# Kernel tuning notes

Measured on AMD Instinct MI355X. Metric: run time of the kernel, lower is better.

Reference implementation:

```python
import jax, jax.numpy as jnp
import numpy as np
from jax import lax

B, T, P, CF, ED, NHID = 32, 8192, 16, 4, 32, 64
CD = ED * (P // CF)            # 128 = code_dim
K, NHEADS, NLAYERS, DFF = 1024, 4, 4, 256
DH = CD // NHEADS
NEG = -1e9


def conv1d(x, w, b, stride=1, pad=0):
    # x: [N, Cin, L], w: [Cout, Cin, k]
    y = lax.conv_general_dilated(x, w, (stride,), [(pad, pad)],
                                 dimension_numbers=("NCH", "OIH", "NCH"))
    return y + b[None, :, None]


def layernorm(x, g, b, eps=1e-5):
    m = jnp.mean(x, -1, keepdims=True)
    v = jnp.mean((x - m) ** 2, -1, keepdims=True)
    return (x - m) * lax.rsqrt(v + eps) * g + b


def setup_inputs() -> dict:
    key = jax.random.key(0)
    ks = iter(jax.random.split(key, 40))
    n = lambda shape, s=0.02: jax.random.normal(next(ks), shape, jnp.float32) * s
    return {
        "x": jax.random.normal(next(ks), (B, T, 1), jnp.float32),
        "enc_w1": n((NHID // 2, 1, 4)), "enc_b1": jnp.zeros((NHID // 2,), jnp.float32),
        "enc_w2": n((NHID, NHID // 2, 4)), "enc_b2": jnp.zeros((NHID,), jnp.float32),
        "enc_w3": n((NHID, NHID, 3)), "enc_b3": jnp.zeros((NHID,), jnp.float32),
        "res_w1": n((2, 32, NHID, 3)), "res_b1": jnp.zeros((2, 32), jnp.float32),
        "res_w2": n((2, NHID, 32, 1)), "res_b2": jnp.zeros((2, NHID), jnp.float32),
        "pre_w": n((ED, NHID, 1)), "pre_b": jnp.zeros((ED,), jnp.float32),
        "codebook": jax.random.uniform(next(ks), (K, CD), jnp.float32, -1.0 / K, 1.0 / K),
        "pos_emb": n((512, CD)),
        "qkv_w": n((NLAYERS, 3 * CD, CD)), "qkv_b": jnp.zeros((NLAYERS, 3 * CD), jnp.float32),
        "proj_w": n((NLAYERS, CD, CD)), "proj_b": jnp.zeros((NLAYERS, CD), jnp.float32),
        "ln1_g": jnp.ones((NLAYERS, CD), jnp.float32), "ln1_b": jnp.zeros((NLAYERS, CD), jnp.float32),
        "ln2_g": jnp.ones((NLAYERS, CD), jnp.float32), "ln2_b": jnp.zeros((NLAYERS, CD), jnp.float32),
        "ffn_w1": n((NLAYERS, DFF, CD)), "ffn_b1": jnp.zeros((NLAYERS, DFF), jnp.float32),
        "ffn_w2": n((NLAYERS, CD, DFF)), "ffn_b2": jnp.zeros((NLAYERS, CD), jnp.float32),
        "fin_g": jnp.ones((CD,), jnp.float32), "fin_b": jnp.zeros((CD,), jnp.float32),
        "head_w": n((K, CD)), "head_b": jnp.zeros((K,), jnp.float32),
    }


def reference(x, enc_w1, enc_b1, enc_w2, enc_b2, enc_w3, enc_b3,
              res_w1, res_b1, res_w2, res_b2, pre_w, pre_b,
              codebook, pos_emb, qkv_w, qkv_b, proj_w, proj_b,
              ln1_g, ln1_b, ln2_g, ln2_b, ffn_w1, ffn_b1, ffn_w2, ffn_b2,
              fin_g, fin_b, head_w, head_b):
    Bx, Tx, C = x.shape
    npatch = Tx // P
    # [B, T, 1] -> patches, channel-major per patch -> [N, 1, P]
    xp = x[:, :npatch * P, :].reshape(Bx, npatch, P, C)
    xp = xp.transpose(0, 1, 3, 2).reshape(-1, 1, P)
    h = jax.nn.relu(conv1d(xp, enc_w1, enc_b1, stride=2, pad=1))
    h = jax.nn.relu(conv1d(h, enc_w2, enc_b2, stride=2, pad=1))
    h = conv1d(h, enc_w3, enc_b3, stride=1, pad=1)
    for i in range(res_w1.shape[0]):           # fixed 2 residual layers
        t = conv1d(jax.nn.relu(h), res_w1[i], res_b1[i], stride=1, pad=1)
        t = conv1d(jax.nn.relu(t), res_w2[i], res_b2[i], stride=1, pad=0)
        h = h + t
    h = jax.nn.relu(h)
    z = conv1d(h, pre_w, pre_b)                # [N, ED, P//CF]
    z_flat = z.reshape(z.shape[0], -1)         # [N, CD]
    # --- flattened VQ: squared-dist + argmin + straight-through ---
    d = (jnp.sum(z_flat ** 2, 1, keepdims=True) + jnp.sum(codebook ** 2, 1)
         - 2.0 * (z_flat @ codebook.T))        # [N, K]
    idx = jnp.argmin(d, axis=1)
    q = codebook[idx]
    sg = lax.stop_gradient
    e_loss = jnp.mean((sg(q) - z_flat) ** 2)
    q_loss = jnp.mean((q - sg(z_flat)) ** 2)
    vq_loss = q_loss + 0.25 * e_loss
    q_st = z_flat + sg(q - z_flat)
    # --- causal transformer over quantized codes ---
    S = npatch
    hh = q_st.reshape(Bx, S, CD) + pos_emb[:S][None]
    mask = jnp.where(jnp.triu(jnp.ones((S, S), bool), k=1), NEG, 0.0).astype(hh.dtype)
    scale = 1.0 / jnp.sqrt(jnp.asarray(DH, hh.dtype))
    for i in range(NLAYERS):
        qkv = hh @ qkv_w[i].T + qkv_b[i]
        qh, kh, vh = [t.reshape(Bx, S, NHEADS, DH) for t in jnp.split(qkv, 3, -1)]
        scores = jnp.einsum("bqhd,bkhd->bhqk", qh, kh) * scale + mask
        attn = jax.nn.softmax(scores, -1)
        o = jnp.einsum("bhqk,bkhd->bqhd", attn, vh).reshape(Bx, S, CD)
        o = o @ proj_w[i].T + proj_b[i]
        hh = layernorm(hh + o, ln1_g[i], ln1_b[i])
        f = jax.nn.gelu(hh @ ffn_w1[i].T + ffn_b1[i], approximate=False)
        f = f @ ffn_w2[i].T + ffn_b2[i]
        hh = layernorm(hh + f, ln2_g[i], ln2_b[i])
    hh = layernorm(hh, fin_g, fin_b)
    logits = hh @ head_w.T + head_b            # [B, S, K]
    return logits, vq_loss, idx.reshape(Bx, S)
```

## Files before the change

kernel.cpp:

```cpp
#include <hip/hip_runtime.h>
#include <math.h>

#define NPATCH 16384
#define SEQ    512
#define LOSS_OFF 16777216
#define IDX_OFF  16777217

typedef short bf8 __attribute__((ext_vector_type(8)));
typedef _Float16 h8 __attribute__((ext_vector_type(8)));
typedef float f32x4 __attribute__((ext_vector_type(4)));

__device__ inline short f2bf(float x) {
  unsigned u = __float_as_uint(x);
  u += 0x7fffu + ((u >> 16) & 1u);
  return (short)(u >> 16);
}
__device__ inline float bf2f(short h) {
  return __uint_as_float(((unsigned)(unsigned short)h) << 16);
}

__device__ inline void splitf16(float v, short& hi, short& lo) {
  _Float16 h = (fabsf(v) < 6.1035156e-5f) ? (_Float16)0.f : (_Float16)v;
  hi = __builtin_bit_cast(short, h);
  lo = __builtin_bit_cast(short, (_Float16)((v - (float)h) * 4096.f));
}

#define EW2_OFF 0
#define EW3_OFF 8192
#define ERA_OFF 20480
#define ERB_OFF 32768
#define EPW_OFF 36864
#define EWTOT   38912

__global__ __launch_bounds__(256) void enc_split(
    const float* __restrict__ w2, const float* __restrict__ w3,
    const float* __restrict__ rw1, const float* __restrict__ rw2,
    const float* __restrict__ pw,
    unsigned short* __restrict__ eh, unsigned short* __restrict__ el) {
  int i = blockIdx.x * 256 + threadIdx.x;
  float v;
  if (i < 8192) {
    int t = i >> 11, co = (i >> 5) & 63, ci = i & 31;
    v = w2[(co * 32 + ci) * 4 + t];
  } else if (i < 20480) {
    int j = i - 8192;
    int t = j >> 12, co = (j >> 6) & 63, ci = j & 63;
    v = w3[(co * 64 + ci) * 3 + t];
  } else if (i < 32768) {
    int j = i - 20480;
    int rl = j / 6144; j -= rl * 6144;
    int t = j >> 11, co = (j >> 6) & 31, ci = j & 63;
    v = rw1[((rl * 32 + co) * 64 + ci) * 3 + t];
  } else if (i < 36864) {
    int j = i - 32768;
    int rl = j >> 11, co = (j >> 5) & 63, ci = j & 31;
    v = rw2[(rl * 64 + co) * 32 + ci];
  } else {
    int j = i - 36864;
    int co = j >> 6, ci = j & 63;
    v = pw[co * 64 + ci];
  }
  short hh_, ll_;
  splitf16(v, hh_, ll_);
  eh[i] = (unsigned short)hh_;
  el[i] = (unsigned short)ll_;
}

__global__ __launch_bounds__(256) void cb_split(
    const float* __restrict__ cb, unsigned short* __restrict__ ch,
    unsigned short* __restrict__ cl, float* __restrict__ cn) {
  const int i = blockIdx.x * 256 + threadIdx.x;
  float v = cb[i];
  short hi, lo;
  splitf16(v * 64.f, hi, lo);
  ch[i] = (unsigned short)hi;
  cl[i] = (unsigned short)lo;
  float s = v * v;
#pragma unroll
  for (int o = 1; o < 64; o <<= 1) s += __shfl_xor(s, o);
  __shared__ float red[4];
  if ((threadIdx.x & 63) == 0) red[threadIdx.x >> 6] = s;
  __syncthreads();
  if (threadIdx.x == 0)   cn[i >> 7] = red[0] + red[1];
  if (threadIdx.x == 128) cn[i >> 7] = red[2] + red[3];
}

#define H1P 2624
#define H2P 2304
__global__ __launch_bounds__(256, 4) void encoder7(
    const float* __restrict__ x,
    const float* __restrict__ w1, const float* __restrict__ b1,
    const float* __restrict__ b2, const float* __restrict__ b3,
    const float* __restrict__ rb1, const float* __restrict__ rb2,
    const float* __restrict__ pb,
    const unsigned short* __restrict__ ewh, const unsigned short* __restrict__ ewl,
    float* __restrict__ z, unsigned short* __restrict__ zh,
    unsigned short* __restrict__ zl) {
  __shared__ __align__(16) short arena[9856];
  short* H1h = arena;
  short* H1l = arena + H1P;
  short* H2h = arena + 2 * H1P;
  short* H2l = arena + 2 * H1P + H2P;
  short* T1h = arena;
  short* T1l = arena + 1280;
  float* XS  = (float*)(arena + 2 * H1P);

  const int tid = threadIdx.x;
  const int wave = tid >> 6, lane = tid & 63, quad = lane >> 4, l15 = lane & 15;
  const int mt = wave >> 1, nh = wave & 1;
  const size_t pbase = (size_t)blockIdx.x * 8;
  const h8 zh8 = {0, 0, 0, 0, 0, 0, 0, 0};
  const f32x4 zf4 = {0.f, 0.f, 0.f, 0.f};

  h8 w2h[4][2], w2l[4][2];
#pragma unroll
  for (int t = 0; t < 4; ++t)
#pragma unroll
    for (int j = 0; j < 2; ++j) {
      const int wb = EW2_OFF + (t * 64 + (nh * 2 + j) * 16 + l15) * 32 + quad * 8;
      w2h[t][j] = *reinterpret_cast<const h8*>(ewh + wb);
      w2l[t][j] = *reinterpret_cast<const h8*>(ewl + wb);
    }

  if (tid < 32) {
    int pp = tid >> 2, i = (tid & 3) * 4;
    *reinterpret_cast<float4*>(&XS[pp * 16 + i]) =
        *reinterpret_cast<const float4*>(x + (pbase + pp) * 16 + i);
  }
  __syncthreads();

  {
    const int pp = tid >> 5, op = (tid >> 2) & 7, qt = tid & 3;
    float xv[4];
#pragma unroll
    for (int kk = 0; kk < 4; ++kk) {
      int ip = 2 * op + kk - 1;
      xv[kk] = (ip >= 0 && ip < 16) ? XS[pp * 16 + ip] : 0.f;
    }
    bf8 sh, sl;
#pragma unroll
    for (int c = 0; c < 8; ++c) {
      int co = qt * 8 + c;
      float4 wv = *reinterpret_cast<const float4*>(w1 + co * 4);
      float a = b1[co] + xv[0] * wv.x + xv[1] * wv.y + xv[2] * wv.z + xv[3] * wv.w;
      a = fmaxf(a, 0.f);
      short hs, ls;
      splitf16(a, hs, ls);
      sh[c] = hs; sl[c] = ls;
    }
    const int off = pp * 328 + op * 40 + qt * 8;
    *reinterpret_cast<bf8*>(&H1h[off]) = sh;
    *reinterpret_cast<bf8*>(&H1l[off]) = sl;
  }
  __syncthreads();

  f32x4 h3keep[2];

  f32x4 acc2A[2] = {zf4, zf4};
  f32x4 acc2B[2] = {zf4, zf4};
  {
    const float bs2_0 = b2[nh * 32 + l15];
    const float bs2_1 = b2[nh * 32 + 16 + l15];
    const int patch = mt * 4 + (l15 >> 2), outp = l15 & 3;
#pragma unroll
    for (int t = 0; t < 4; ++t) {
      const int ip = 2 * outp + t - 1;
      const bool vld = (unsigned)ip < 8u;
      const int aoff = patch * 328 + (vld ? ip : 0) * 40 + quad * 8;
      h8 ah = *reinterpret_cast<const h8*>(&H1h[aoff]);
      h8 al = *reinterpret_cast<const h8*>(&H1l[aoff]);
      if (!vld) { ah = zh8; al = zh8; }
#pragma unroll
      for (int j = 0; j < 2; ++j) {
        acc2A[j] = __builtin_amdgcn_mfma_f32_16x16x32_f16(ah, w2h[t][j], acc2A[j], 0, 0, 0);
        acc2B[j] = __builtin_amdgcn_mfma_f32_16x16x32_f16(ah, w2l[t][j], acc2B[j], 0, 0, 0);
        acc2B[j] = __builtin_amdgcn_mfma_f32_16x16x32_f16(al, w2h[t][j], acc2B[j], 0, 0, 0);
      }
    }
    h8 w3h[3][2][2], w3l[3][2][2];
#pragma unroll
    for (int t = 0; t < 3; ++t)
#pragma unroll
      for (int ks = 0; ks < 2; ++ks)
#pragma unroll
        for (int j = 0; j < 2; ++j) {
          const int wb = EW3_OFF + (t * 64 + (nh * 2 + j) * 16 + l15) * 64 + ks * 32 + quad * 8;
          w3h[t][ks][j] = *reinterpret_cast<const h8*>(ewh + wb);
          w3l[t][ks][j] = *reinterpret_cast<const h8*>(ewl + wb);
        }
#pragma unroll
    for (int j = 0; j < 2; ++j) {
      const int col = (nh * 2 + j) * 16 + l15;
      const float bs = (j == 0) ? bs2_0 : bs2_1;
#pragma unroll
      for (int r = 0; r < 4; ++r) {
        float v = fmaxf(acc2A[j][r] + acc2B[j][r] * (1.f / 4096.f) + bs, 0.f);
        short vh, vl;
        splitf16(v, vh, vl);
        const int m = mt * 16 + quad * 4 + r;
        H2h[m * 72 + col] = vh;
        H2l[m * 72 + col] = vl;
      }
    }
    __syncthreads();

    f32x4 accA[2] = {zf4, zf4};
    f32x4 accB[2] = {zf4, zf4};
    const float bs3_0 = b3[nh * 32 + l15];
    const float bs3_1 = b3[nh * 32 + 16 + l15];
    const int pos = l15 & 3;
#pragma unroll
    for (int t = 0; t < 3; ++t) {
      const int ip = pos + t - 1;
      const bool vld = (unsigned)ip < 4u;
      const int row = patch * 4 + (vld ? ip : 0);
#pragma unroll
      for (int ks = 0; ks < 2; ++ks) {
        const int aoff = row * 72 + ks * 32 + quad * 8;
        h8 ah = *reinterpret_cast<const h8*>(&H2h[aoff]);
        h8 al = *reinterpret_cast<const h8*>(&H2l[aoff]);
        if (!vld) { ah = zh8; al = zh8; }
#pragma unroll
        for (int j = 0; j < 2; ++j) {
          accA[j] = __builtin_amdgcn_mfma_f32_16x16x32_f16(ah, w3h[t][ks][j], accA[j], 0, 0, 0);
          accB[j] = __builtin_amdgcn_mfma_f32_16x16x32_f16(ah, w3l[t][ks][j], accB[j], 0, 0, 0);
          accB[j] = __builtin_amdgcn_mfma_f32_16x16x32_f16(al, w3h[t][ks][j], accB[j], 0, 0, 0);
        }
      }
    }
    __syncthreads();
#pragma unroll
    for (int j = 0; j < 2; ++j) {
      const int col = (nh * 2 + j) * 16 + l15;
      const float bs = (j == 0) ? bs3_0 : bs3_1;
#pragma unroll
      for (int r = 0; r < 4; ++r) {
        float v = accA[j][r] + accB[j][r] * (1.f / 4096.f) + bs;
        h3keep[j][r] = v;
        short vh, vl;
        splitf16(fmaxf(v, 0.f), vh, vl);
        const int m = mt * 16 + quad * 4 + r;
        H2h[m * 72 + col] = vh;
        H2l[m * 72 + col] = vl;
      }
    }
  }
  __syncthreads();

  for (int rl = 0; rl < 2; ++rl) {
    {
      h8 wah[3][2], wal[3][2];
#pragma unroll
      for (int t = 0; t < 3; ++t)
#pragma unroll
        for (int ks = 0; ks < 2; ++ks) {
          const int wb = ERA_OFF + ((rl * 3 + t) * 32 + nh * 16 + l15) * 64 + ks * 32 + quad * 8;
          wah[t][ks] = *reinterpret_cast<const h8*>(ewh + wb);
          wal[t][ks] = *reinterpret_cast<const h8*>(ewl + wb);
        }
      const float bsa = rb1[rl * 32 + nh * 16 + l15];
      f32x4 accA = zf4, accB = zf4;
      const int patch = mt * 4 + (l15 >> 2), pos = l15 & 3;
#pragma unroll
      for (int t = 0; t < 3; ++t) {
        const int ip = pos + t - 1;
        const bool vld = (unsigned)ip < 4u;
        const int row = patch * 4 + (vld ? ip : 0);
#pragma unroll
        for (int ks = 0; ks < 2; ++ks) {
          const int aoff = row * 72 + ks * 32 + quad * 8;
          h8 ah = *reinterpret_cast<const h8*>(&H2h[aoff]);
          h8 al = *reinterpret_cast<const h8*>(&H2l[aoff]);
          if (!vld) { ah = zh8; al = zh8; }
          accA = __builtin_amdgcn_mfma_f32_16x16x32_f16(ah, wah[t][ks], accA, 0, 0, 0);
          accB = __builtin_amdgcn_mfma_f32_16x16x32_f16(ah, wal[t][ks], accB, 0, 0, 0);
          accB = __builtin_amdgcn_mfma_f32_16x16x32_f16(al, wah[t][ks], accB, 0, 0, 0);
        }
      }
      const int col = nh * 16 + l15;
#pragma unroll
      for (int r = 0; r < 4; ++r) {
        float v = fmaxf(accA[r] + accB[r] * (1.f / 4096.f) + bsa, 0.f);
        short vh, vl;
        splitf16(v, vh, vl);
        const int m = mt * 16 + quad * 4 + r;
        T1h[m * 40 + col] = vh;
        T1l[m * 40 + col] = vl;
      }
    }
    __syncthreads();
    {
      h8 wbh[2], wbl[2];
#pragma unroll
      for (int j = 0; j < 2; ++j) {
        const int wb = ERB_OFF + (rl * 64 + (nh * 2 + j) * 16 + l15) * 32 + quad * 8;
        wbh[j] = *reinterpret_cast<const h8*>(ewh + wb);
        wbl[j] = *reinterpret_cast<const h8*>(ewl + wb);
      }
      const float bsb0 = rb2[rl * 64 + nh * 32 + l15];
      const float bsb1 = rb2[rl * 64 + nh * 32 + 16 + l15];
      f32x4 accA[2] = {zf4, zf4};
      f32x4 accB[2] = {zf4, zf4};
      const int aoff = (mt * 16 + l15) * 40 + quad * 8;
      h8 ah = *reinterpret_cast<const h8*>(&T1h[aoff]);
      h8 al = *reinterpret_cast<const h8*>(&T1l[aoff]);
#pragma unroll
      for (int j = 0; j < 2; ++j) {
        accA[j] = __builtin_amdgcn_mfma_f32_16x16x32_f16(ah, wbh[j], accA[j], 0, 0, 0);
        accB[j] = __builtin_amdgcn_mfma_f32_16x16x32_f16(ah, wbl[j], accB[j], 0, 0, 0);
        accB[j] = __builtin_amdgcn_mfma_f32_16x16x32_f16(al, wbh[j], accB[j], 0, 0, 0);
      }
#pragma unroll
      for (int j = 0; j < 2; ++j) {
        const int col = (nh * 2 + j) * 16 + l15;
        const float bs = (j == 0) ? bsb0 : bsb1;
#pragma unroll
        for (int r = 0; r < 4; ++r) {
          float v = h3keep[j][r] + accA[j][r] + accB[j][r] * (1.f / 4096.f) + bs;
          h3keep[j][r] = v;
          short vh, vl;
          splitf16(fmaxf(v, 0.f), vh, vl);
          const int m = mt * 16 + quad * 4 + r;
          H2h[m * 72 + col] = vh;
          H2l[m * 72 + col] = vl;
        }
      }
    }
    __syncthreads();
  }

  {
    h8 wph[2], wpl[2];
#pragma unroll
    for (int ks = 0; ks < 2; ++ks) {
      const int wb = EPW_OFF + (nh * 16 + l15) * 64 + ks * 32 + quad * 8;
      wph[ks] = *reinterpret_cast<const h8*>(ewh + wb);
      wpl[ks] = *reinterpret_cast<const h8*>(ewl + wb);
    }
    const float bs = pb[nh * 16 + l15];
    f32x4 accA = zf4, accB = zf4;
    const int arow = mt * 16 + l15;
#pragma unroll
    for (int ks = 0; ks < 2; ++ks) {
      const int aoff = arow * 72 + ks * 32 + quad * 8;
      h8 ah = *reinterpret_cast<const h8*>(&H2h[aoff]);
      h8 al = *reinterpret_cast<const h8*>(&H2l[aoff]);
      accA = __builtin_amdgcn_mfma_f32_16x16x32_f16(ah, wph[ks], accA, 0, 0, 0);
      accB = __builtin_amdgcn_mfma_f32_16x16x32_f16(ah, wpl[ks], accB, 0, 0, 0);
      accB = __builtin_amdgcn_mfma_f32_16x16x32_f16(al, wph[ks], accB, 0, 0, 0);
    }
    const int pn = mt * 4 + quad;
    const int col = nh * 16 + l15;
    float ov[4];
#pragma unroll
    for (int r = 0; r < 4; ++r) ov[r] = accA[r] + accB[r] * (1.f / 4096.f) + bs;
    const size_t off = (pbase + pn) * 128 + col * 4;
    *reinterpret_cast<float4*>(z + off) = *reinterpret_cast<float4*>(ov);
    ushort4 h4, l4;
    unsigned short* hp = (unsigned short*)&h4;
    unsigned short* lp = (unsigned short*)&l4;
#pragma unroll
    for (int r = 0; r < 4; ++r) {
      short vh, vl;
      splitf16(ov[r] * 256.f, vh, vl);
      hp[r] = (unsigned short)vh;
      lp[r] = (unsigned short)vl;
    }
    *reinterpret_cast<ushort4*>(&zh[off]) = h4;
    *reinterpret_cast<ushort4*>(&zl[off]) = l4;
  }
}

__global__ __launch_bounds__(256) void cast_w(
    const float* __restrict__ qkv_w, const float* __restrict__ proj_w,
    const float* __restrict__ f1, const float* __restrict__ f2,
    const float* __restrict__ hw, unsigned short* __restrict__ wb) {
  int i = blockIdx.x * 256 + threadIdx.x;
  float v;
  if (i < 196608) v = qkv_w[i];
  else if (i < 262144) v = proj_w[i - 196608];
  else if (i < 393216) v = f1[i - 262144];
  else if (i < 524288) v = f2[i - 393216];
  else v = hw[i - 524288];
  wb[i] = (unsigned short)f2bf(v);
}

__global__ __launch_bounds__(256) void vq_argmin3(
    const unsigned short* __restrict__ Ahg, const unsigned short* __restrict__ Alg,
    const unsigned short* __restrict__ Bhg, const unsigned short* __restrict__ Blg,
    const float* __restrict__ cbf, unsigned long long* __restrict__ keys) {
  __shared__ short Ah[128 * 40], Al[128 * 40], Bh[64 * 40], Bl[64 * 40];
  __shared__ float cns[64];
  const int tid = threadIdx.x;
  const int n0 = blockIdx.x * 64, m0 = blockIdx.y * 128;
  const int wave = tid >> 6, lane = tid & 63, quad = lane >> 4, l15 = lane & 15;
  const f32x4 z4 = {0.f, 0.f, 0.f, 0.f};
  f32x4 accA[2][4], accB[2][4];
#pragma unroll
  for (int i = 0; i < 2; ++i)
#pragma unroll
    for (int j = 0; j < 4; ++j) { accA[i][j] = z4; accB[i][j] = z4; }
  {
    const int lr = tid >> 2, q = tid & 3;
    const float4* bp = reinterpret_cast<const float4*>(cbf + (size_t)(n0 + lr) * 128 + q * 32);
    float s = 0.f;
#pragma unroll
    for (int e = 0; e < 8; ++e) {
      float4 v = bp[e];
      s += v.x * v.x + v.y * v.y + v.z * v.z + v.w * v.w;
    }
    s += __shfl_xor(s, 1); s += __shfl_xor(s, 2);
    if (q == 0) cns[lr] = s;
  }
  const int ra = tid >> 1, ha = (tid & 1) * 16;
  const int rb = tid >> 2, hb = (tid & 3) * 8;
  for (int k0 = 0; k0 < 128; k0 += 32) {
    {
      const size_t abase = (size_t)(m0 + ra) * 128 + k0 + ha;
      *reinterpret_cast<bf8*>(&Ah[ra * 40 + ha])     = *reinterpret_cast<const bf8*>(&Ahg[abase]);
      *reinterpret_cast<bf8*>(&Ah[ra * 40 + ha + 8]) = *reinterpret_cast<const bf8*>(&Ahg[abase + 8]);
      *reinterpret_cast<bf8*>(&Al[ra * 40 + ha])     = *reinterpret_cast<const bf8*>(&Alg[abase]);
      *reinterpret_cast<bf8*>(&Al[ra * 40 + ha + 8]) = *reinterpret_cast<const bf8*>(&Alg[abase + 8]);
      const size_t bbase = (size_t)(n0 + rb) * 128 + k0 + hb;
      *reinterpret_cast<bf8*>(&Bh[rb * 40 + hb]) = *reinterpret_cast<const bf8*>(&Bhg[bbase]);
      *reinterpret_cast<bf8*>(&Bl[rb * 40 + hb]) = *reinterpret_cast<const bf8*>(&Blg[bbase]);
    }
    __syncthreads();
    h8 af[2], afl[2], bfh[4], bfl[4];
#pragma unroll
    for (int mt = 0; mt < 2; ++mt) {
      int row = wave * 32 + mt * 16 + l15;
      af[mt]  = *reinterpret_cast<const h8*>(&Ah[row * 40 + quad * 8]);
      afl[mt] = *reinterpret_cast<const h8*>(&Al[row * 40 + quad * 8]);
    }
#pragma unroll
    for (int nt = 0; nt < 4; ++nt) {
      int row = nt * 16 + l15;
      bfh[nt] = *reinterpret_cast<const h8*>(&Bh[row * 40 + quad * 8]);
      bfl[nt] = *reinterpret_cast<const h8*>(&Bl[row * 40 + quad * 8]);
    }
#pragma unroll
    for (int nt = 0; nt < 4; ++nt)
#pragma unroll
      for (int mt = 0; mt < 2; ++mt) {
        accA[mt][nt] = __builtin_amdgcn_mfma_f32_16x16x32_f16(af[mt], bfh[nt], accA[mt][nt], 0, 0, 0);
        accB[mt][nt] = __builtin_amdgcn_mfma_f32_16x16x32_f16(af[mt], bfl[nt], accB[mt][nt], 0, 0, 0);
        accB[mt][nt] = __builtin_amdgcn_mfma_f32_16x16x32_f16(afl[mt], bfh[nt], accB[mt][nt], 0, 0, 0);
      }
    __syncthreads();
  }
#pragma unroll
  for (int mt = 0; mt < 2; ++mt)
#pragma unroll
    for (int r = 0; r < 4; ++r) {
      const int row = m0 + wave * 32 + mt * 16 + quad * 4 + r;
      unsigned long long key = ~0ull;
#pragma unroll
      for (int nt = 0; nt < 4; ++nt) {
        const int c16 = nt * 16 + l15;
        float s = (accA[mt][nt][r] + accB[mt][nt][r] * (1.f / 4096.f)) * (1.f / 16384.f);
        float dv = cns[c16] - 2.f * s;
        unsigned u = __float_as_uint(dv);
        u = (u & 0x80000000u) ? ~u : (u | 0x80000000u);
        unsigned long long k = ((unsigned long long)u << 32) | (unsigned)(n0 + c16);
        key = k < key ? k : key;
      }
#pragma unroll
      for (int off = 1; off < 16; off <<= 1) {
        unsigned long long o = __shfl_xor(key, off);
        key = o < key ? o : key;
      }
      if (l15 == 0) atomicMin(&keys[row], key);
    }
}

__global__ __launch_bounds__(256) void vq_gather3(
    const float* __restrict__ z, const float* __restrict__ cb,
    const float* __restrict__ pos, const unsigned long long* __restrict__ keys,
    float* __restrict__ hh, unsigned short* __restrict__ hh_b,
    float* __restrict__ lpart, float* __restrict__ idx_out) {
  const int blk = blockIdx.x, tid = threadIdx.x;
  __shared__ int sidx[8];
  if (tid < 8) {
    unsigned long long k = keys[blk * 8 + tid];
    int id = (int)(unsigned)(k & 0xffffffffull);
    sidx[tid] = id;
    idx_out[blk * 8 + tid] = (float)id;
  }
  __syncthreads();
  const int p = tid >> 5, d = tid & 31;
  const size_t n = (size_t)blk * 8 + p;
  const int idx = sidx[p];
  float4 q = *reinterpret_cast<const float4*>(cb + (size_t)idx * 128 + d * 4);
  float4 zv = *reinterpret_cast<const float4*>(z + n * 128 + d * 4);
  float4 pv = *reinterpret_cast<const float4*>(pos + (size_t)(n & 511) * 128 + d * 4);
  float hv[4] = {q.x + pv.x, q.y + pv.y, q.z + pv.z, q.w + pv.w};
  *reinterpret_cast<float4*>(hh + n * 128 + d * 4) = *reinterpret_cast<float4*>(hv);
  ushort4 h4;
  unsigned short* hp = (unsigned short*)&h4;
#pragma unroll
  for (int e = 0; e < 4; ++e) hp[e] = (unsigned short)f2bf(hv[e]);
  *reinterpret_cast<ushort4*>(&hh_b[n * 128 + d * 4]) = h4;
  float dx = q.x - zv.x, dy = q.y - zv.y, dz = q.z - zv.z, dw = q.w - zv.w;
  float part = dx * dx + dy * dy + dz * dz + dw * dw;
#pragma unroll
  for (int o = 1; o < 64; o <<= 1) part += __shfl_xor(part, o);
  __shared__ float lred[4];
  if ((tid & 63) == 0) lred[tid >> 6] = part;
  __syncthreads();
  if (tid == 0) lpart[blk] = lred[0] + lred[1] + lred[2] + lred[3];
}

template <int ACT, int SPLIT>
__global__ __launch_bounds__(256) void mgemm_b64(
    const unsigned short* __restrict__ Ag, const unsigned short* __restrict__ Bg,
    const float* __restrict__ bias, float* __restrict__ C,
    unsigned short* __restrict__ Cb, int N) {
  __shared__ short Ah[64 * 40], Bh[64 * 40];
  const int tid = threadIdx.x;
  const int n0 = blockIdx.x * 64, m0 = blockIdx.y * 64;
  const int wave = tid >> 6, lane = tid & 63, quad = lane >> 4, l15 = lane & 15;
  const f32x4 z4 = {0.f, 0.f, 0.f, 0.f};
  f32x4 acc[4] = {z4, z4, z4, z4};

  const int ra = tid >> 2, ha = (tid & 3) * 8;
  for (int k0 = 0; k0 < 128; k0 += 32) {
    *reinterpret_cast<bf8*>(&Ah[ra * 40 + ha]) =
        *reinterpret_cast<const bf8*>(&Ag[(size_t)(m0 + ra) * 128 + k0 + ha]);
    *reinterpret_cast<bf8*>(&Bh[ra * 40 + ha]) =
        *reinterpret_cast<const bf8*>(&Bg[(size_t)(n0 + ra) * 128 + k0 + ha]);
    __syncthreads();
    bf8 af = *reinterpret_cast<const bf8*>(&Ah[(wave * 16 + l15) * 40 + quad * 8]);
    bf8 bfh[4];
#pragma unroll
    for (int nt = 0; nt < 4; ++nt)
      bfh[nt] = *reinterpret_cast<const bf8*>(&Bh[(nt * 16 + l15) * 40 + quad * 8]);
#pragma unroll
    for (int nt = 0; nt < 4; ++nt)
      acc[nt] = __builtin_amdgcn_mfma_f32_16x16x32_bf16(af, bfh[nt], acc[nt], 0, 0, 0);
    __syncthreads();
  }
#pragma unroll
  for (int nt = 0; nt < 4; ++nt) {
    int col = n0 + nt * 16 + l15;
    float bv = bias[col];
    int rbase = m0 + wave * 16 + quad * 4;
#pragma unroll
    for (int r = 0; r < 4; ++r) {
      float v = acc[nt][r] + bv;
      if (ACT == 1) v = 0.5f * v * (1.f + erff(v * 0.7071067811865476f));
      if (SPLIT) Cb[(size_t)(rbase + r) * N + col] = (unsigned short)f2bf(v);
      else       C[(size_t)(rbase + r) * N + col] = v;
    }
  }
}

template <int K, int FINAL>
__global__ __launch_bounds__(256) void mgemm_ln3(
    const unsigned short* __restrict__ Ag, const unsigned short* __restrict__ Bg,
    const float* __restrict__ bias, const float* __restrict__ res,
    const float* __restrict__ g, const float* __restrict__ bb,
    const float* __restrict__ g2, const float* __restrict__ bb2,
    float* __restrict__ C, unsigned short* __restrict__ Cb) {
  __shared__ short Ah[16 * 40], Bh[128 * 40];
  __shared__ float red1[16][4], red2[16][4], red3[16][4], red4[16][4];
  const int tid = threadIdx.x;
  const int m0 = blockIdx.x * 16;
  const int wave = tid >> 6, lane = tid & 63, quad = lane >> 4, l15 = lane & 15;
  const f32x4 z4 = {0.f, 0.f, 0.f, 0.f};
  f32x4 acc[2] = {z4, z4};

  const int rb = tid >> 1, hb = (tid & 1) * 16;
  for (int k0 = 0; k0 < K; k0 += 32) {
    if (tid < 64) {
      const int ra = tid >> 2, ha = (tid & 3) * 8;
      *reinterpret_cast<bf8*>(&Ah[ra * 40 + ha]) =
          *reinterpret_cast<const bf8*>(&Ag[(size_t)(m0 + ra) * K + k0 + ha]);
    }
    {
      const size_t bbase = (size_t)rb * K + k0 + hb;
      *reinterpret_cast<bf8*>(&Bh[rb * 40 + hb])     = *reinterpret_cast<const bf8*>(&Bg[bbase]);
      *reinterpret_cast<bf8*>(&Bh[rb * 40 + hb + 8]) = *reinterpret_cast<const bf8*>(&Bg[bbase + 8]);
    }
    __syncthreads();
    bf8 af = *reinterpret_cast<const bf8*>(&Ah[l15 * 40 + quad * 8]);
#pragma unroll
    for (int j = 0; j < 2; ++j) {
      bf8 bf = *reinterpret_cast<const bf8*>(&Bh[(wave * 32 + j * 16 + l15) * 40 + quad * 8]);
      acc[j] = __builtin_amdgcn_mfma_f32_16x16x32_bf16(af, bf, acc[j], 0, 0, 0);
    }
    __syncthreads();
  }
  float bias_v[2], g_v[2], bb_v[2], g2_v[2], bb2_v[2];
#pragma unroll
  for (int j = 0; j < 2; ++j) {
    const int col = wave * 32 + j * 16 + l15;
    bias_v[j] = bias[col]; g_v[j] = g[col]; bb_v[j] = bb[col];
    if (FINAL) { g2_v[j] = g2[col]; bb2_v[j] = bb2[col]; }
  }
  float ov[4][2];
#pragma unroll
  for (int r = 0; r < 4; ++r) {
    const int row = m0 + quad * 4 + r;
#pragma unroll
    for (int j = 0; j < 2; ++j)
      ov[r][j] = acc[j][r] + bias_v[j] +
                 res[(size_t)row * 128 + wave * 32 + j * 16 + l15];
    float s = ov[r][0] + ov[r][1];
    s += __shfl_xor(s, 1); s += __shfl_xor(s, 2);
    s += __shfl_xor(s, 4); s += __shfl_xor(s, 8);
    if (l15 == 0) red1[quad * 4 + r][wave] = s;
  }
  __syncthreads();
  float mean[4];
#pragma unroll
  for (int r = 0; r < 4; ++r) {
    const int lr = quad * 4 + r;
    mean[r] = (red1[lr][0] + red1[lr][1] + red1[lr][2] + red1[lr][3]) * 0.0078125f;
  }
#pragma unroll
  for (int r = 0; r < 4; ++r) {
    float s2 = 0.f;
#pragma unroll
    for (int j = 0; j < 2; ++j) { ov[r][j] -= mean[r]; s2 += ov[r][j] * ov[r][j]; }
    s2 += __shfl_xor(s2, 1); s2 += __shfl_xor(s2, 2);
    s2 += __shfl_xor(s2, 4); s2 += __shfl_xor(s2, 8);
    if (l15 == 0) red2[quad * 4 + r][wave] = s2;
  }
  __syncthreads();
  float rstd[4];
#pragma unroll
  for (int r = 0; r < 4; ++r) {
    const int lr = quad * 4 + r;
    rstd[r] = rsqrtf((red2[lr][0] + red2[lr][1] + red2[lr][2] + red2[lr][3]) *
                     0.0078125f + 1e-5f);
  }
  if (FINAL) {
    float yv[4][2];
#pragma unroll
    for (int r = 0; r < 4; ++r) {
      float s3 = 0.f;
#pragma unroll
      for (int j = 0; j < 2; ++j) {
        yv[r][j] = ov[r][j] * rstd[r] * g_v[j] + bb_v[j];
        s3 += yv[r][j];
      }
      s3 += __shfl_xor(s3, 1); s3 += __shfl_xor(s3, 2);
      s3 += __shfl_xor(s3, 4); s3 += __shfl_xor(s3, 8);
      if (l15 == 0) red3[quad * 4 + r][wave] = s3;
    }
    __syncthreads();
    float mean2[4];
#pragma unroll
    for (int r = 0; r < 4; ++r) {
      const int lr = quad * 4 + r;
      mean2[r] = (red3[lr][0] + red3[lr][1] + red3[lr][2] + red3[lr][3]) * 0.0078125f;
    }
#pragma unroll
    for (int r = 0; r < 4; ++r) {
      float s4 = 0.f;
#pragma unroll
      for (int j = 0; j < 2; ++j) { yv[r][j] -= mean2[r]; s4 += yv[r][j] * yv[r][j]; }
      s4 += __shfl_xor(s4, 1); s4 += __shfl_xor(s4, 2);
      s4 += __shfl_xor(s4, 4); s4 += __shfl_xor(s4, 8);
      if (l15 == 0) red4[quad * 4 + r][wave] = s4;
    }
    __syncthreads();
#pragma unroll
    for (int r = 0; r < 4; ++r) {
      const int lr = quad * 4 + r;
      float rstd2 = rsqrtf((red4[lr][0] + red4[lr][1] + red4[lr][2] + red4[lr][3]) *
                           0.0078125f + 1e-5f);
      const int row = m0 + lr;
#pragma unroll
      for (int j = 0; j < 2; ++j) {
        float v = yv[r][j] * rstd2 * g2_v[j] + bb2_v[j];
        Cb[(size_t)row * 128 + wave * 32 + j * 16 + l15] = (unsigned short)f2bf(v);
      }
    }
  } else {
#pragma unroll
    for (int r = 0; r < 4; ++r) {
      const int row = m0 + quad * 4 + r;
#pragma unroll
      for (int j = 0; j < 2; ++j) {
        float v = ov[r][j] * rstd[r] * g_v[j] + bb_v[j];
        size_t off = (size_t)row * 128 + wave * 32 + j * 16 + l15;
        C[off] = v;
        Cb[off] = (unsigned short)f2bf(v);
      }
    }
  }
}

__global__ __launch_bounds__(256) void attn_b(
    const unsigned short* __restrict__ qb, unsigned short* __restrict__ ob) {
  const int qt = blockIdx.x, h = blockIdx.y, b = blockIdx.z;
  __shared__ short Kh[64 * 40];
  __shared__ short Vth[32 * 72];
  __shared__ float Ss[64 * 72];
  __shared__ float ms[64], ls[64], alphas[64];
  const int tid = threadIdx.x;
  const int wave = tid >> 6, lane = tid & 63, quad = lane >> 4, l15 = lane & 15;
  const size_t tbase = (size_t)b * 512 + qt * 64;
  bf8 qf;
  {
    const size_t qoff = (tbase + wave * 16 + l15) * 384 + h * 32 + quad * 8;
    qf = *reinterpret_cast<const bf8*>(&qb[qoff]);
  }
  if (tid < 64) { ms[tid] = -1e30f; ls[tid] = 0.f; }
  const f32x4 z4 = {0.f, 0.f, 0.f, 0.f};
  f32x4 o[2] = {z4, z4};
  const float scale = 0.17677669529663687f;
  const int sr = tid >> 2, sc8 = (tid & 3) * 8;
  for (int kt = 0; kt <= qt; ++kt) {
    const size_t kbase = (size_t)b * 512 + kt * 64;
    {
      const size_t koff = (kbase + sr) * 384 + 128 + h * 32 + sc8;
      *reinterpret_cast<bf8*>(&Kh[sr * 40 + sc8]) = *reinterpret_cast<const bf8*>(&qb[koff]);
      const size_t voff = (kbase + sr) * 384 + 256 + h * 32 + sc8;
      bf8 vh8 = *reinterpret_cast<const bf8*>(&qb[voff]);
#pragma unroll
      for (int j = 0; j < 8; ++j) Vth[(sc8 + j) * 72 + sr] = vh8[j];
    }
    __syncthreads();
    {
#pragma unroll
      for (int nt = 0; nt < 4; ++nt) {
        bf8 kf = *reinterpret_cast<const bf8*>(&Kh[(nt * 16 + l15) * 40 + quad * 8]);
        f32x4 s = __builtin_amdgcn_mfma_f32_16x16x32_bf16(qf, kf, z4, 0, 0, 0);
#pragma unroll
        for (int r = 0; r < 4; ++r) {
          int row64 = wave * 16 + quad * 4 + r;
          int col64 = nt * 16 + l15;
          float v = s[r] * scale;
          if (kt == qt && col64 > row64) v += -1e9f;
          Ss[row64 * 72 + col64] = v;
        }
      }
    }
    __syncthreads();
    {
      const int i = tid >> 2, q = tid & 3;
      float mx = -3.4e38f;
      float4 pv[4];
#pragma unroll
      for (int t = 0; t < 4; ++t) {
        pv[t] = *reinterpret_cast<const float4*>(&Ss[i * 72 + q * 16 + t * 4]);
        mx = fmaxf(mx, fmaxf(fmaxf(pv[t].x, pv[t].y), fmaxf(pv[t].z, pv[t].w)));
      }
      mx = fmaxf(mx, __shfl_xor(mx, 1));
      mx = fmaxf(mx, __shfl_xor(mx, 2));
      float mold = ms[i];
      mx = fmaxf(mx, mold);
      float sum = 0.f;
#pragma unroll
      for (int t = 0; t < 4; ++t) {
        pv[t].x = __expf(pv[t].x - mx); pv[t].y = __expf(pv[t].y - mx);
        pv[t].z = __expf(pv[t].z - mx); pv[t].w = __expf(pv[t].w - mx);
        sum += pv[t].x + pv[t].y + pv[t].z + pv[t].w;
        *reinterpret_cast<float4*>(&Ss[i * 72 + q * 16 + t * 4]) = pv[t];
      }
      sum += __shfl_xor(sum, 1);
      sum += __shfl_xor(sum, 2);
      if (q == 0) {
        float alpha = __expf(mold - mx);
        ls[i] = ls[i] * alpha + sum;
        ms[i] = mx;
        alphas[i] = alpha;
      }
    }
    __syncthreads();
    {
      bf8 ph[2];
#pragma unroll
      for (int c = 0; c < 2; ++c) {
        const float* pp = &Ss[(wave * 16 + l15) * 72 + c * 32 + quad * 8];
        float4 p0 = *reinterpret_cast<const float4*>(pp);
        float4 p1 = *reinterpret_cast<const float4*>(pp + 4);
        float pf[8] = {p0.x, p0.y, p0.z, p0.w, p1.x, p1.y, p1.z, p1.w};
#pragma unroll
        for (int j = 0; j < 8; ++j) ph[c][j] = f2bf(pf[j]);
      }
      float a0 = alphas[wave * 16 + quad * 4 + 0];
      float a1 = alphas[wave * 16 + quad * 4 + 1];
      float a2 = alphas[wave * 16 + quad * 4 + 2];
      float a3 = alphas[wave * 16 + quad * 4 + 3];
#pragma unroll
      for (int dt = 0; dt < 2; ++dt) {
        o[dt][0] *= a0; o[dt][1] *= a1; o[dt][2] *= a2; o[dt][3] *= a3;
#pragma unroll
        for (int c = 0; c < 2; ++c) {
          bf8 vf = *reinterpret_cast<const bf8*>(&Vth[(dt * 16 + l15) * 72 + c * 32 + quad * 8]);
          o[dt] = __builtin_amdgcn_mfma_f32_16x16x32_bf16(ph[c], vf, o[dt], 0, 0, 0);
        }
      }
    }
    __syncthreads();
  }
#pragma unroll
  for (int r = 0; r < 4; ++r) {
    float inv = 1.f / ls[wave * 16 + quad * 4 + r];
    size_t row = tbase + wave * 16 + quad * 4 + r;
#pragma unroll
    for (int dt = 0; dt < 2; ++dt) {
      float v = o[dt][r] * inv;
      ob[row * 128 + h * 32 + dt * 16 + l15] = (unsigned short)f2bf(v);
    }
  }
}

__global__ __launch_bounds__(256) void loss_finalize2(const float* __restrict__ lp,
                                                      float* __restrict__ out) {
  float s = 0.f;
  for (int i = threadIdx.x; i < 2048; i += 256) s += lp[i];
#pragma unroll
  for (int o = 1; o < 64; o <<= 1) s += __shfl_xor(s, o);
  __shared__ float red[4];
  if ((threadIdx.x & 63) == 0) red[threadIdx.x >> 6] = s;
  __syncthreads();
  if (threadIdx.x == 0)
    out[0] = 1.25f * (red[0] + red[1] + red[2] + red[3]) / 2097152.0f;
}

extern "C" void kernel_launch(void* const* d_in, const int* in_sizes, int n_in,
                              void* d_out, int out_size, void* d_ws, size_t ws_size,
                              hipStream_t stream) {
  const float* x      = (const float*)d_in[0];
  const float* enc_w1 = (const float*)d_in[1];
  const float* enc_b1 = (const float*)d_in[2];
  const float* enc_w2 = (const float*)d_in[3];
  const float* enc_b2 = (const float*)d_in[4];
  const float* enc_w3 = (const float*)d_in[5];
  const float* enc_b3 = (const float*)d_in[6];
  const float* res_w1 = (const float*)d_in[7];
  const float* res_b1 = (const float*)d_in[8];
  const float* res_w2 = (const float*)d_in[9];
  const float* res_b2 = (const float*)d_in[10];
  const float* pre_w  = (const float*)d_in[11];
  const float* pre_b  = (const float*)d_in[12];
  const float* codebook = (const float*)d_in[13];
  const float* pos_emb  = (const float*)d_in[14];
  const float* qkv_w  = (const float*)d_in[15];
  const float* qkv_b  = (const float*)d_in[16];
  const float* proj_w = (const float*)d_in[17];
  const float* proj_b = (const float*)d_in[18];
  const float* ln1_g  = (const float*)d_in[19];
  const float* ln1_b  = (const float*)d_in[20];
  const float* ln2_g  = (const float*)d_in[21];
  const float* ln2_b  = (const float*)d_in[22];
  const float* ffn_w1 = (const float*)d_in[23];
  const float* ffn_b1 = (const float*)d_in[24];
  const float* ffn_w2 = (const float*)d_in[25];
  const float* ffn_b2 = (const float*)d_in[26];
  const float* fin_g  = (const float*)d_in[27];
  const float* fin_b  = (const float*)d_in[28];
  const float* head_w = (const float*)d_in[29];
  const float* head_b = (const float*)d_in[30];

  float* out = (float*)d_out;
  float* ws  = (float*)d_ws;

  unsigned long long* keys = (unsigned long long*)ws;
  float* lpart = ws + 32768;
  unsigned short* wb = (unsigned short*)(ws + 36864);
  unsigned short* hhln_b = (unsigned short*)(ws + 692224);

  float* zf = out;
  float* hh = out + 2097152;
  unsigned short* hh_b   = (unsigned short*)(out + 4194304);
  unsigned short* qkvb_b = (unsigned short*)(out + 6291456);
  unsigned short* oatt_b = (unsigned short*)(out + 12582912);
  unsigned short* fbuf_b = (unsigned short*)(out + 0);

  unsigned short* ewh = (unsigned short*)(out + 6291456);
  unsigned short* ewl = ewh + EWTOT;

  unsigned short* zh = (unsigned short*)(out + 6340608);
  unsigned short* zl = (unsigned short*)(out + 7389184);
  unsigned short* cbh = (unsigned short*)(out + 12582912);
  unsigned short* cbl = (unsigned short*)(out + 12648448);
  float* cnbuf = out + 12713984;

  const int W_QKV = 0, W_PROJ = 196608, W_F1 = 262144, W_F2 = 393216, W_HEAD = 524288;

  hipMemsetAsync(keys, 0xFF, NPATCH * sizeof(unsigned long long), stream);

  enc_split<<<152, 256, 0, stream>>>(enc_w2, enc_w3, res_w1, res_w2, pre_w, ewh, ewl);
  cb_split<<<512, 256, 0, stream>>>(codebook, cbh, cbl, cnbuf);
  encoder7<<<2048, 256, 0, stream>>>(x, enc_w1, enc_b1, enc_b2, enc_b3,
                                     res_b1, res_b2, pre_b, ewh, ewl, zf, zh, zl);
  cast_w<<<2304, 256, 0, stream>>>(qkv_w, proj_w, ffn_w1, ffn_w2, head_w, wb);
  vq_argmin3<<<dim3(16, 128), 256, 0, stream>>>(zh, zl, cbh, cbl, codebook, keys);
  vq_gather3<<<2048, 256, 0, stream>>>(zf, codebook, pos_emb, keys, hh, hh_b,
                                       lpart, out + IDX_OFF);
  for (int i = 0; i < 4; ++i) {
    mgemm_b64<0, 1><<<dim3(6, 256), 256, 0, stream>>>(
        hh_b, wb + W_QKV + i * 49152, qkv_b + i * 384, nullptr, qkvb_b, 384);
    attn_b<<<dim3(8, 4, 32), 256, 0, stream>>>(qkvb_b, oatt_b);
    mgemm_ln3<128, 0><<<1024, 256, 0, stream>>>(
        oatt_b, wb + W_PROJ + i * 16384, proj_b + i * 128, hh,
        ln1_g + i * 128, ln1_b + i * 128, nullptr, nullptr, hh, hh_b);
    mgemm_b64<1, 1><<<dim3(4, 256), 256, 0, stream>>>(
        hh_b, wb + W_F1 + i * 32768, ffn_b1 + i * 256, nullptr, fbuf_b, 256);
    if (i < 3) {
      mgemm_ln3<256, 0><<<1024, 256, 0, stream>>>(
          fbuf_b, wb + W_F2 + i * 32768, ffn_b2 + i * 128, hh,
          ln2_g + i * 128, ln2_b + i * 128, nullptr, nullptr, hh, hh_b);
    } else {
      mgemm_ln3<256, 1><<<1024, 256, 0, stream>>>(
          fbuf_b, wb + W_F2 + i * 32768, ffn_b2 + i * 128, hh,
          ln2_g + i * 128, ln2_b + i * 128, fin_g, fin_b, hh, hhln_b);
    }
  }
  mgemm_b64<0, 0><<<dim3(16, 256), 256, 0, stream>>>(
      hhln_b, wb + W_HEAD, head_b, out, nullptr, 1024);
  loss_finalize2<<<1, 256, 0, stream>>>(lpart, out + LOSS_OFF);
}
```

Measured before the change: 538.8 us.

## Fuse FFN up/down GEMMs with LayerNorm and merge prep kernels

Replaces the separate FFN1 GEMM (with GELU) and FFN2+LayerNorm kernels with one kernel. Each 64-row tile keeps the GELU intermediate in shared memory, so the 256-wide activation never goes through global memory. It also folds the encoder weight split, codebook split, weight cast and key memset into one prep launch, and replaces the final loss reduction kernel with atomicAdd into the output. This cuts launches and global traffic, at the cost of fewer blocks per FFN launch (256), higher LDS use per block, and nondeterministic float atomic ordering in the loss.

```diff
diff --git a/kernel.cpp b/kernel.cpp
--- a/kernel.cpp
+++ b/kernel.cpp
@@ -32,57 +32,75 @@
 #define EPW_OFF 36864
 #define EWTOT   38912
 
-__global__ __launch_bounds__(256) void enc_split(
+__global__ __launch_bounds__(256) void prep_all(
     const float* __restrict__ w2, const float* __restrict__ w3,
     const float* __restrict__ rw1, const float* __restrict__ rw2,
-    const float* __restrict__ pw,
-    unsigned short* __restrict__ eh, unsigned short* __restrict__ el) {
-  int i = blockIdx.x * 256 + threadIdx.x;
-  float v;
-  if (i < 8192) {
-    int t = i >> 11, co = (i >> 5) & 63, ci = i & 31;
-    v = w2[(co * 32 + ci) * 4 + t];
-  } else if (i < 20480) {
-    int j = i - 8192;
-    int t = j >> 12, co = (j >> 6) & 63, ci = j & 63;
-    v = w3[(co * 64 + ci) * 3 + t];
-  } else if (i < 32768) {
-    int j = i - 20480;
-    int rl = j / 6144; j -= rl * 6144;
-    int t = j >> 11, co = (j >> 6) & 31, ci = j & 63;
-    v = rw1[((rl * 32 + co) * 64 + ci) * 3 + t];
-  } else if (i < 36864) {
-    int j = i - 32768;
-    int rl = j >> 11, co = (j >> 5) & 63, ci = j & 31;
-    v = rw2[(rl * 64 + co) * 32 + ci];
+    const float* __restrict__ pw, const float* __restrict__ cb,
+    const float* __restrict__ qkv_w, const float* __restrict__ proj_w,
+    const float* __restrict__ f1, const float* __restrict__ f2,
+    const float* __restrict__ hw,
+    unsigned short* __restrict__ eh, unsigned short* __restrict__ el,
+    unsigned short* __restrict__ cbh, unsigned short* __restrict__ cbl,
+    float* __restrict__ cn, unsigned short* __restrict__ wb,
+    unsigned long long* __restrict__ keys, float* __restrict__ loss_out) {
+  __shared__ float red[4];
+  const int b = blockIdx.x, tid = threadIdx.x;
+  if (b < 152) {
+    int i = b * 256 + tid;
+    float v;
+    if (i < 8192) {
+      int t = i >> 11, co = (i >> 5) & 63, ci = i & 31;
+      v = w2[(co * 32 + ci) * 4 + t];
+    } else if (i < 20480) {
+      int j = i - 8192;
+      int t = j >> 12, co = (j >> 6) & 63, ci = j & 63;
+      v = w3[(co * 64 + ci) * 3 + t];
+    } else if (i < 32768) {
+      int j = i - 20480;
+      int rl = j / 6144; j -= rl * 6144;
+      int t = j >> 11, co = (j >> 6) & 31, ci = j & 63;
+      v = rw1[((rl * 32 + co) * 64 + ci) * 3 + t];
+    } else if (i < 36864) {
+      int j = i - 32768;
+      int rl = j >> 11, co = (j >> 5) & 63, ci = j & 31;
+      v = rw2[(rl * 64 + co) * 32 + ci];
+    } else {
+      int j = i - 36864;
+      int co = j >> 6, ci = j & 63;
+      v = pw[co * 64 + ci];
+    }
+    short hh_, ll_;
+    splitf16(v, hh_, ll_);
+    eh[i] = (unsigned short)hh_;
+    el[i] = (unsigned short)ll_;
+  } else if (b < 664) {
+    const int i = (b - 152) * 256 + tid;
+    float v = cb[i];
+    short hi, lo;
+    splitf16(v * 64.f, hi, lo);
+    cbh[i] = (unsigned short)hi;
+    cbl[i] = (unsigned short)lo;
+    float s = v * v;
+#pragma unroll
+    for (int o = 1; o < 64; o <<= 1) s += __shfl_xor(s, o);
+    if ((tid & 63) == 0) red[tid >> 6] = s;
+    __syncthreads();
+    if (tid == 0)   cn[i >> 7] = red[0] + red[1];
+    if (tid == 128) cn[i >> 7] = red[2] + red[3];
+  } else if (b < 2968) {
+    int i = (b - 664) * 256 + tid;
+    float v;
+    if (i < 196608) v = qkv_w[i];
+    else if (i < 262144) v = proj_w[i - 196608];
+    else if (i < 393216) v = f1[i - 262144];
+    else if (i < 524288) v = f2[i - 393216];
+    else v = hw[i - 524288];
+    wb[i] = (unsigned short)f2bf(v);
   } else {
-    int j = i - 36864;
-    int co = j >> 6, ci = j & 63;
-    v = pw[co * 64 + ci];
-  }
-  short hh_, ll_;
-  splitf16(v, hh_, ll_);
-  eh[i] = (unsigned short)hh_;
-  el[i] = (unsigned short)ll_;
-}
-
-__global__ __launch_bounds__(256) void cb_split(
-    const float* __restrict__ cb, unsigned short* __restrict__ ch,
-    unsigned short* __restrict__ cl, float* __restrict__ cn) {
-  const int i = blockIdx.x * 256 + threadIdx.x;
-  float v = cb[i];
-  short hi, lo;
-  splitf16(v * 64.f, hi, lo);
-  ch[i] = (unsigned short)hi;
-  cl[i] = (unsigned short)lo;
-  float s = v * v;
-#pragma unroll
-  for (int o = 1; o < 64; o <<= 1) s += __shfl_xor(s, o);
-  __shared__ float red[4];
-  if ((threadIdx.x & 63) == 0) red[threadIdx.x >> 6] = s;
-  __syncthreads();
-  if (threadIdx.x == 0)   cn[i >> 7] = red[0] + red[1];
-  if (threadIdx.x == 128) cn[i >> 7] = red[2] + red[3];
+    int i = (b - 2968) * 256 + tid;
+    keys[i] = ~0ull;
+    if (b == 2968 && tid == 0) loss_out[0] = 0.f;
+  }
 }
 
 #define H1P 2624
@@ -371,20 +389,6 @@
   }
 }
 
-__global__ __launch_bounds__(256) void cast_w(
-    const float* __restrict__ qkv_w, const float* __restrict__ proj_w,
-    const float* __restrict__ f1, const float* __restrict__ f2,
-    const float* __restrict__ hw, unsigned short* __restrict__ wb) {
-  int i = blockIdx.x * 256 + threadIdx.x;
-  float v;
-  if (i < 196608) v = qkv_w[i];
-  else if (i < 262144) v = proj_w[i - 196608];
-  else if (i < 393216) v = f1[i - 262144];
-  else if (i < 524288) v = f2[i - 393216];
-  else v = hw[i - 524288];
-  wb[i] = (unsigned short)f2bf(v);
-}
-
 __global__ __launch_bounds__(256) void vq_argmin3(
     const unsigned short* __restrict__ Ahg, const unsigned short* __restrict__ Alg,
     const unsigned short* __restrict__ Bhg, const unsigned short* __restrict__ Blg,
@@ -478,7 +482,7 @@
     const float* __restrict__ z, const float* __restrict__ cb,
     const float* __restrict__ pos, const unsigned long long* __restrict__ keys,
     float* __restrict__ hh, unsigned short* __restrict__ hh_b,
-    float* __restrict__ lpart, float* __restrict__ idx_out) {
+    float* __restrict__ loss_out, float* __restrict__ idx_out) {
   const int blk = blockIdx.x, tid = threadIdx.x;
   __shared__ int sidx[8];
   if (tid < 8) {
@@ -508,7 +512,9 @@
   __shared__ float lred[4];
   if ((tid & 63) == 0) lred[tid >> 6] = part;
   __syncthreads();
-  if (tid == 0) lpart[blk] = lred[0] + lred[1] + lred[2] + lred[3];
+  if (tid == 0)
+    atomicAdd(loss_out,
+              1.25f * (lred[0] + lred[1] + lred[2] + lred[3]) / 2097152.0f);
 }
 
 template <int ACT, int SPLIT>
@@ -563,7 +569,7 @@
     const float* __restrict__ g2, const float* __restrict__ bb2,
     float* __restrict__ C, unsigned short* __restrict__ Cb) {
   __shared__ short Ah[16 * 40], Bh[128 * 40];
-  __shared__ float red1[16][4], red2[16][4], red3[16][4], red4[16][4];
+  __shared__ float red1[16][4], red2[16][4];
   const int tid = threadIdx.x;
   const int m0 = blockIdx.x * 16;
   const int wave = tid >> 6, lane = tid & 63, quad = lane >> 4, l15 = lane & 15;
@@ -636,6 +642,7 @@
                      0.0078125f + 1e-5f);
   }
   if (FINAL) {
+    __shared__ float red3[16][4], red4[16][4];
     float yv[4][2];
 #pragma unroll
     for (int r = 0; r < 4; ++r) {
@@ -686,6 +693,135 @@
       for (int j = 0; j < 2; ++j) {
         float v = ov[r][j] * rstd[r] * g_v[j] + bb_v[j];
         size_t off = (size_t)row * 128 + wave * 32 + j * 16 + l15;
+        C[off] = v;
+        Cb[off] = (unsigned short)f2bf(v);
+      }
+    }
+  }
+}
+
+template <int FINAL>
+__global__ __launch_bounds__(256) void ffn_fused(
+    const unsigned short* __restrict__ Ag, const unsigned short* __restrict__ W1g,
+    const unsigned short* __restrict__ W2g,
+    const float* __restrict__ b1v, const float* __restrict__ b2v,
+    const float* __restrict__ res,
+    const float* __restrict__ g, const float* __restrict__ bb,
+    const float* __restrict__ g2, const float* __restrict__ bb2,
+    float* __restrict__ C, unsigned short* __restrict__ Cb) {
+  __shared__ __align__(16) short arena[22016];
+  short* Ah  = arena;
+  short* W1s = arena + 2560;
+  short* F   = arena;
+  short* W2s = arena + 16896;
+  const int tid = threadIdx.x;
+  const int m0 = blockIdx.x * 64;
+  const int wave = tid >> 6, lane = tid & 63, quad = lane >> 4, l15 = lane & 15;
+  const f32x4 z4 = {0.f, 0.f, 0.f, 0.f};
+
+  f32x4 acc1[16];
+#pragma unroll
+  for (int nt = 0; nt < 16; ++nt) acc1[nt] = z4;
+  const int ra = tid >> 2, ha = (tid & 3) * 8;
+  for (int k0 = 0; k0 < 128; k0 += 32) {
+    *reinterpret_cast<bf8*>(&Ah[ra * 40 + ha]) =
+        *reinterpret_cast<const bf8*>(&Ag[(size_t)(m0 + ra) * 128 + k0 + ha]);
+#pragma unroll
+    for (int q = 0; q < 4; ++q)
+      *reinterpret_cast<bf8*>(&W1s[tid * 40 + q * 8]) =
+          *reinterpret_cast<const bf8*>(&W1g[(size_t)tid * 128 + k0 + q * 8]);
+    __syncthreads();
+    bf8 af = *reinterpret_cast<const bf8*>(&Ah[(wave * 16 + l15) * 40 + quad * 8]);
+#pragma unroll
+    for (int nt = 0; nt < 16; ++nt) {
+      bf8 bf = *reinterpret_cast<const bf8*>(&W1s[(nt * 16 + l15) * 40 + quad * 8]);
+      acc1[nt] = __builtin_amdgcn_mfma_f32_16x16x32_bf16(af, bf, acc1[nt], 0, 0, 0);
+    }
+    __syncthreads();
+  }
+#pragma unroll
+  for (int nt = 0; nt < 16; ++nt) {
+    const int col = nt * 16 + l15;
+    const float bv = b1v[col];
+#pragma unroll
+    for (int r = 0; r < 4; ++r) {
+      float v = acc1[nt][r] + bv;
+      v = 0.5f * v * (1.f + erff(v * 0.7071067811865476f));
+      F[(wave * 16 + quad * 4 + r) * 264 + col] = f2bf(v);
+    }
+  }
+  __syncthreads();
+
+  f32x4 acc[8];
+#pragma unroll
+  for (int j = 0; j < 8; ++j) acc[j] = z4;
+  const int rw = tid >> 1, hw = (tid & 1) * 16;
+  for (int k0 = 0; k0 < 256; k0 += 32) {
+    {
+      const size_t wbase = (size_t)rw * 256 + k0 + hw;
+      *reinterpret_cast<bf8*>(&W2s[rw * 40 + hw])     = *reinterpret_cast<const bf8*>(&W2g[wbase]);
+      *reinterpret_cast<bf8*>(&W2s[rw * 40 + hw + 8]) = *reinterpret_cast<const bf8*>(&W2g[wbase + 8]);
+    }
+    __syncthreads();
+    bf8 ff = *reinterpret_cast<const bf8*>(&F[(wave * 16 + l15) * 264 + k0 + quad * 8]);
+#pragma unroll
+    for (int nt = 0; nt < 8; ++nt) {
+      bf8 wf = *reinterpret_cast<const bf8*>(&W2s[(nt * 16 + l15) * 40 + quad * 8]);
+      acc[nt] = __builtin_amdgcn_mfma_f32_16x16x32_bf16(ff, wf, acc[nt], 0, 0, 0);
+    }
+    __syncthreads();
+  }
+  float bias_v[8], g_v[8], bb_v[8], g2_v[8], bb2_v[8];
+#pragma unroll
+  for (int nt = 0; nt < 8; ++nt) {
+    int col = nt * 16 + l15;
+    bias_v[nt] = b2v[col]; g_v[nt] = g[col]; bb_v[nt] = bb[col];
+    if (FINAL) { g2_v[nt] = g2[col]; bb2_v[nt] = bb2[col]; }
+  }
+  const int rbase = m0 + wave * 16 + quad * 4;
+#pragma unroll
+  for (int r = 0; r < 4; ++r) {
+    const int row = rbase + r;
+    float ov[8];
+    float s = 0.f;
+#pragma unroll
+    for (int nt = 0; nt < 8; ++nt) {
+      ov[nt] = acc[nt][r] + bias_v[nt] + res[(size_t)row * 128 + nt * 16 + l15];
+      s += ov[nt];
+    }
+    s += __shfl_xor(s, 1); s += __shfl_xor(s, 2);
+    s += __shfl_xor(s, 4); s += __shfl_xor(s, 8);
+    float mean = s * 0.0078125f;
+    float s2 = 0.f;
+#pragma unroll
+    for (int nt = 0; nt < 8; ++nt) { ov[nt] -= mean; s2 += ov[nt] * ov[nt]; }
+    s2 += __shfl_xor(s2, 1); s2 += __shfl_xor(s2, 2);
+    s2 += __shfl_xor(s2, 4); s2 += __shfl_xor(s2, 8);
+    float rstd = rsqrtf(s2 * 0.0078125f + 1e-5f);
+    if (FINAL) {
+      float yv[8];
+      float s3 = 0.f;
+#pragma unroll
+      for (int nt = 0; nt < 8; ++nt) { yv[nt] = ov[nt] * rstd * g_v[nt] + bb_v[nt]; s3 += yv[nt]; }
+      s3 += __shfl_xor(s3, 1); s3 += __shfl_xor(s3, 2);
+      s3 += __shfl_xor(s3, 4); s3 += __shfl_xor(s3, 8);
+      float mean2 = s3 * 0.0078125f;
+      float s4 = 0.f;
+#pragma unroll
+      for (int nt = 0; nt < 8; ++nt) { yv[nt] -= mean2; s4 += yv[nt] * yv[nt]; }
+      s4 += __shfl_xor(s4, 1); s4 += __shfl_xor(s4, 2);
+      s4 += __shfl_xor(s4, 4); s4 += __shfl_xor(s4, 8);
+      float rstd2 = rsqrtf(s4 * 0.0078125f + 1e-5f);
+#pragma unroll
+      for (int nt = 0; nt < 8; ++nt) {
+        float v = yv[nt] * rstd2 * g2_v[nt] + bb2_v[nt];
+        Cb[(size_t)row * 128 + nt * 16 + l15] = (unsigned short)f2bf(v);
+      }
+    } else {
+#pragma unroll
+      for (int nt = 0; nt < 8; ++nt) {
+        float v = ov[nt] * rstd * g_v[nt] + bb_v[nt];
+        size_t off = (size_t)row * 128 + nt * 16 + l15;
         C[off] = v;
         Cb[off] = (unsigned short)f2bf(v);
       }
@@ -808,19 +944,6 @@
       ob[row * 128 + h * 32 + dt * 16 + l15] = (unsigned short)f2bf(v);
     }
   }
-}
-
-__global__ __launch_bounds__(256) void loss_finalize2(const float* __restrict__ lp,
-                                                      float* __restrict__ out) {
-  float s = 0.f;
-  for (int i = threadIdx.x; i < 2048; i += 256) s += lp[i];
-#pragma unroll
-  for (int o = 1; o < 64; o <<= 1) s += __shfl_xor(s, o);
-  __shared__ float red[4];
-  if ((threadIdx.x & 63) == 0) red[threadIdx.x >> 6] = s;
-  __syncthreads();
-  if (threadIdx.x == 0)
-    out[0] = 1.25f * (red[0] + red[1] + red[2] + red[3]) / 2097152.0f;
 }
 
 extern "C" void kernel_launch(void* const* d_in, const int* in_sizes, int n_in,
@@ -862,7 +985,6 @@
   float* ws  = (float*)d_ws;
 
   unsigned long long* keys = (unsigned long long*)ws;
-  float* lpart = ws + 32768;
   unsigned short* wb = (unsigned short*)(ws + 36864);
   unsigned short* hhln_b = (unsigned short*)(ws + 692224);
 
@@ -871,7 +993,6 @@
   unsigned short* hh_b   = (unsigned short*)(out + 4194304);
   unsigned short* qkvb_b = (unsigned short*)(out + 6291456);
   unsigned short* oatt_b = (unsigned short*)(out + 12582912);
-  unsigned short* fbuf_b = (unsigned short*)(out + 0);
 
   unsigned short* ewh = (unsigned short*)(out + 6291456);
   unsigned short* ewl = ewh + EWTOT;
@@ -884,16 +1005,15 @@
 
   const int W_QKV = 0, W_PROJ = 196608, W_F1 = 262144, W_F2 = 393216, W_HEAD = 524288;
 
-  hipMemsetAsync(keys, 0xFF, NPATCH * sizeof(unsigned long long), stream);
-
-  enc_split<<<152, 256, 0, stream>>>(enc_w2, enc_w3, res_w1, res_w2, pre_w, ewh, ewl);
-  cb_split<<<512, 256, 0, stream>>>(codebook, cbh, cbl, cnbuf);
+  prep_all<<<3032, 256, 0, stream>>>(
+      enc_w2, enc_w3, res_w1, res_w2, pre_w, codebook,
+      qkv_w, proj_w, ffn_w1, ffn_w2, head_w,
+      ewh, ewl, cbh, cbl, cnbuf, wb, keys, out + LOSS_OFF);
   encoder7<<<2048, 256, 0, stream>>>(x, enc_w1, enc_b1, enc_b2, enc_b3,
                                      res_b1, res_b2, pre_b, ewh, ewl, zf, zh, zl);
-  cast_w<<<2304, 256, 0, stream>>>(qkv_w, proj_w, ffn_w1, ffn_w2, head_w, wb);
   vq_argmin3<<<dim3(16, 128), 256, 0, stream>>>(zh, zl, cbh, cbl, codebook, keys);
   vq_gather3<<<2048, 256, 0, stream>>>(zf, codebook, pos_emb, keys, hh, hh_b,
-                                       lpart, out + IDX_OFF);
+                                       out + LOSS_OFF, out + IDX_OFF);
   for (int i = 0; i < 4; ++i) {
     mgemm_b64<0, 1><<<dim3(6, 256), 256, 0, stream>>>(
         hh_b, wb + W_QKV + i * 49152, qkv_b + i * 384, nullptr, qkvb_b, 384);
@@ -901,19 +1021,18 @@
     mgemm_ln3<128, 0><<<1024, 256, 0, stream>>>(
         oatt_b, wb + W_PROJ + i * 16384, proj_b + i * 128, hh,
         ln1_g + i * 128, ln1_b + i * 128, nullptr, nullptr, hh, hh_b);
-    mgemm_b64<1, 1><<<dim3(4, 256), 256, 0, stream>>>(
-        hh_b, wb + W_F1 + i * 32768, ffn_b1 + i * 256, nullptr, fbuf_b, 256);
     if (i < 3) {
-      mgemm_ln3<256, 0><<<1024, 256, 0, stream>>>(
-          fbuf_b, wb + W_F2 + i * 32768, ffn_b2 + i * 128, hh,
+      ffn_fused<0><<<256, 256, 0, stream>>>(
+          hh_b, wb + W_F1 + i * 32768, wb + W_F2 + i * 32768,
+          ffn_b1 + i * 256, ffn_b2 + i * 128, hh,
           ln2_g + i * 128, ln2_b + i * 128, nullptr, nullptr, hh, hh_b);
     } else {
-      mgemm_ln3<256, 1><<<1024, 256, 0, stream>>>(
-          fbuf_b, wb + W_F2 + i * 32768, ffn_b2 + i * 128, hh,
+      ffn_fused<1><<<256, 256, 0, stream>>>(
+          hh_b, wb + W_F1 + i * 32768, wb + W_F2 + i * 32768,
+          ffn_b1 + i * 256, ffn_b2 + i * 128, hh,
           ln2_g + i * 128, ln2_b + i * 128, fin_g, fin_b, hh, hhln_b);
     }
   }
   mgemm_b64<0, 0><<<dim3(16, 256), 256, 0, stream>>>(
       hhln_b, wb + W_HEAD, head_b, out, nullptr, 1024);
-  loss_finalize2<<<1, 256, 0, stream>>>(lpart, out + LOSS_OFF);
-}
+}
```

Result: slower. 623.9 us (+15.8%).
